# Optimization experiments

Hardware: AMD Instinct MI355X
Metric: run time of the kernel (lower is better)

Reference implementation:

```python
import jax, jax.numpy as jnp
import numpy as np

EMB = 1024
HEADS = 16
HEAD_DIM = EMB // HEADS


def setup_inputs() -> dict:
    key = jax.random.key(0)
    ks = jax.random.split(key, 12)
    B, S = 4, 2048
    scale = 1.0 / np.sqrt(EMB)
    inp = {
        'values': jax.random.normal(ks[0], (B, S, EMB), jnp.float32),
        'keys': jax.random.normal(ks[1], (B, S, EMB), jnp.float32),
        'query': jax.random.normal(ks[2], (B, S, EMB), jnp.float32),
        'Wv': jax.random.normal(ks[3], (EMB, EMB), jnp.float32) * scale,
        'bv': jnp.zeros((EMB,), jnp.float32),
        'Wk': jax.random.normal(ks[4], (EMB, EMB), jnp.float32) * scale,
        'bk': jnp.zeros((EMB,), jnp.float32),
        'Wq': jax.random.normal(ks[5], (EMB, EMB), jnp.float32) * scale,
        'bq': jnp.zeros((EMB,), jnp.float32),
        'Wo': jax.random.normal(ks[6], (EMB, EMB), jnp.float32) * scale,
        'bo': jnp.zeros((EMB,), jnp.float32),
    }
    return inp


def reference(values, keys, query, Wv, bv, Wk, bk, Wq, bq, Wo, bo):
    B, S, _ = values.shape
    # Linear projections (torch Linear: x @ W.T + b)
    v = values @ Wv.T + bv
    k = keys @ Wk.T + bk
    q = query @ Wq.T + bq
    # Reshape to (B, S, H, D) -- NOTE: original does NOT transpose heads,
    # so attention is computed across the HEAD axis per position.
    v = v.reshape(B, S, HEADS, HEAD_DIM)
    k = k.reshape(B, S, HEADS, HEAD_DIM)
    q = q.reshape(B, S, HEADS, HEAD_DIM)
    # (B,S,H,D) @ (B,S,D,H) -> (B,S,H,H) head-head scores
    scores = jnp.einsum('bshd,bsgd->bshg', q, k) * (HEAD_DIM ** -0.5)
    attn = jax.nn.softmax(scores, axis=-1)
    # (B,S,H,H) @ (B,S,H,D) -> (B,S,H,D)
    out = jnp.einsum('bshg,bsgd->bshd', attn, v)
    out = out.reshape(B, S, EMB)
    return out @ Wo.T + bo
```

## Files before the change

### kernel.cpp

```cpp
#include <hip/hip_runtime.h>
#include <stdint.h>

#define EMB 1024
#define LROW 40

typedef unsigned short u16;
typedef __attribute__((ext_vector_type(8))) unsigned short u16x8;
typedef __attribute__((ext_vector_type(8))) __bf16 bf16x8;
typedef __attribute__((ext_vector_type(4))) float f32x4;

__device__ __forceinline__ u16 f2bf(float f) {
  union { float f; uint32_t u; } x; x.f = f;
  uint32_t u = x.u;
  u += 0x7fff + ((u >> 16) & 1u);
  return (u16)(u >> 16);
}

__device__ __forceinline__ bf16x8 cvt8(float4 a, float4 b) {
  bf16x8 r;
  r[0] = (__bf16)a.x; r[1] = (__bf16)a.y; r[2] = (__bf16)a.z; r[3] = (__bf16)a.w;
  r[4] = (__bf16)b.x; r[5] = (__bf16)b.y; r[6] = (__bf16)b.z; r[7] = (__bf16)b.w;
  return r;
}

__device__ __forceinline__ void gl16(const u16* g, u16* l) {
  __builtin_amdgcn_global_load_lds(
      (const __attribute__((address_space(1))) void*)g,
      (__attribute__((address_space(3))) void*)l, 16, 0, 0);
}

__device__ __forceinline__ int xcd_logical(int orig, int nwg) {
  return (orig & 7) * (nwg >> 3) + (orig >> 3);
}

__global__ __launch_bounds__(256) void cvtw_kernel(
    const float* __restrict__ s0, u16* __restrict__ d0,
    const float* __restrict__ s1, u16* __restrict__ d1,
    const float* __restrict__ s2, u16* __restrict__ d2,
    const float* __restrict__ s3, u16* __restrict__ d3)
{
  const float* s; u16* d;
  switch (blockIdx.y) {
    case 0:  s = s0; d = d0; break;
    case 1:  s = s1; d = d1; break;
    case 2:  s = s2; d = d2; break;
    default: s = s3; d = d3; break;
  }
  const size_t i = (size_t)blockIdx.x * 256 + threadIdx.x;
  const float4* f = (const float4*)(s + i * 8);
  const float4 lo = f[0], hi = f[1];
  *(bf16x8*)(d + i * 8) = cvt8(lo, hi);
}

__global__ __launch_bounds__(256, 3) void qkv_fused_kernel(
    const float* __restrict__ Vx, const float* __restrict__ Kx,
    const float* __restrict__ Qx, const u16* __restrict__ Wb,
    const float* __restrict__ Bv, const float* __restrict__ Bk,
    const float* __restrict__ Bq,
    u16* __restrict__ cv, u16* __restrict__ ck, u16* __restrict__ cq,
    int N, int K, int M)
{
  __shared__ __attribute__((aligned(16))) u16 Al[2][128 * 32];
  __shared__ __attribute__((aligned(16))) u16 Bl[2][128 * 32];

  const int nwg = (N >> 7) * (M >> 7) * 3;
  const int logical = xcd_logical(blockIdx.x, nwg);
  const int per_z = (N >> 7) * (M >> 7);
  const int z = logical / per_z;
  const int rem = logical - z * per_z;
  const int nbx = N >> 7;
  const int by = rem / nbx, bx = rem - by * nbx;

  const float* X; const u16* W; const float* Bias; u16* C;
  switch (z) {
    case 0:  X = Vx; W = Wb;                   Bias = Bv; C = cv; break;
    case 1:  X = Kx; W = Wb + EMB * EMB;       Bias = Bk; C = ck; break;
    default: X = Qx; W = Wb + 2 * EMB * EMB;   Bias = Bq; C = cq; break;
  }

  const int tid  = threadIdx.x;
  const int lane = tid & 63;
  const int w    = tid >> 6;
  const int wm = w >> 1, wn = w & 1;
  const int r16 = lane & 15, quad = lane >> 4;
  const int bm = by * 128, bn = bx * 128;

  const int s0 = tid, s1 = tid + 256;
  const int r0 = s0 >> 2, c0 = s0 & 3;
  const int r1 = s1 >> 2, c1 = s1 & 3;
  const int lA0 = r0 * 32 + ((c0 ^ ((r0 >> 1) & 3)) * 8);
  const int lA1 = r1 * 32 + ((c1 ^ ((r1 >> 1) & 3)) * 8);
  const size_t xo0 = (size_t)(bm + r0) * K + c0 * 8;
  const size_t xo1 = (size_t)(bm + r1) * K + c1 * 8;

  const int bs0 = w * 64 + lane, bs1 = bs0 + 256;
  const int br0 = bs0 >> 2, bc0 = ((bs0 & 3) ^ ((br0 >> 1) & 3)) * 8;
  const int br1 = bs1 >> 2, bc1 = ((bs1 & 3) ^ ((br1 >> 1) & 3)) * 8;
  const u16* srcB0 = W + (size_t)(bn + br0) * K + bc0;
  const u16* srcB1 = W + (size_t)(bn + br1) * K + bc1;
  const int dB0o = (w * 64) * 8, dB1o = dB0o + 256 * 8;

  const int swz = (quad ^ ((r16 >> 1) & 3)) * 8;
  int offA[4], offB[4];
#pragma unroll
  for (int t = 0; t < 4; t++) {
    offA[t] = (wm * 64 + t * 16 + r16) * 32 + swz;
    offB[t] = (wn * 64 + t * 16 + r16) * 32 + swz;
  }

  f32x4 acc[4][4];
#pragma unroll
  for (int i = 0; i < 4; i++)
#pragma unroll
    for (int j = 0; j < 4; j++)
      acc[i][j] = f32x4{0.f, 0.f, 0.f, 0.f};

  float4 xa0 = *(const float4*)(X + xo0), xa1 = *(const float4*)(X + xo0 + 4);
  float4 xb0 = *(const float4*)(X + xo1), xb1 = *(const float4*)(X + xo1 + 4);
  *(bf16x8*)&Al[0][lA0] = cvt8(xa0, xa1);
  *(bf16x8*)&Al[0][lA1] = cvt8(xb0, xb1);
  gl16(srcB0, &Bl[0][dB0o]);
  gl16(srcB1, &Bl[0][dB1o]);
  __builtin_amdgcn_sched_barrier(0);
  xa0 = *(const float4*)(X + xo0 + 32); xa1 = *(const float4*)(X + xo0 + 36);
  xb0 = *(const float4*)(X + xo1 + 32); xb1 = *(const float4*)(X + xo1 + 36);
  asm volatile("s_waitcnt vmcnt(4) lgkmcnt(0)\n\ts_barrier" ::: "memory");

  for (int k0 = 0; k0 < K; k0 += 32) {
    const int cur = (k0 >> 5) & 1, nxt = cur ^ 1;
    const int kn  = (k0 + 32) & (K - 1);
    const int kn2 = (k0 + 64) & (K - 1);

    *(bf16x8*)&Al[nxt][lA0] = cvt8(xa0, xa1);
    *(bf16x8*)&Al[nxt][lA1] = cvt8(xb0, xb1);
    gl16(srcB0 + kn, &Bl[nxt][dB0o]);
    gl16(srcB1 + kn, &Bl[nxt][dB1o]);
    __builtin_amdgcn_sched_barrier(0);
    xa0 = *(const float4*)(X + xo0 + kn2); xa1 = *(const float4*)(X + xo0 + kn2 + 4);
    xb0 = *(const float4*)(X + xo1 + kn2); xb1 = *(const float4*)(X + xo1 + kn2 + 4);

    bf16x8 a[4], b[4];
#pragma unroll
    for (int t = 0; t < 4; t++) a[t] = *(const bf16x8*)&Al[cur][offA[t]];
#pragma unroll
    for (int t = 0; t < 4; t++) b[t] = *(const bf16x8*)&Bl[cur][offB[t]];
    asm volatile("s_waitcnt lgkmcnt(0)" ::: "memory");
    __builtin_amdgcn_sched_barrier(0);

#pragma unroll
    for (int tm = 0; tm < 4; tm++)
#pragma unroll
      for (int tn = 0; tn < 4; tn++)
        acc[tm][tn] = __builtin_amdgcn_mfma_f32_16x16x32_bf16(a[tm], b[tn], acc[tm][tn], 0, 0, 0);

    asm volatile("s_waitcnt vmcnt(4)\n\ts_barrier" ::: "memory");
  }

#pragma unroll
  for (int tn = 0; tn < 4; tn++) {
    const int col = bn + wn * 64 + tn * 16 + r16;
    const float bias = Bias[col];
#pragma unroll
    for (int tm = 0; tm < 4; tm++) {
      const int row0 = bm + wm * 64 + tm * 16 + quad * 4;
#pragma unroll
      for (int r = 0; r < 4; r++)
        C[(size_t)(row0 + r) * N + col] = f2bf(acc[tm][tn][r] + bias);
    }
  }
}

__global__ __launch_bounds__(256, 3) void out_gemm_kernel(
    const u16* __restrict__ X, const u16* __restrict__ W,
    const float* __restrict__ Bias, float* __restrict__ C, int N, int K, int M)
{
  __shared__ __attribute__((aligned(16))) u16 Al[2][128 * 32];
  __shared__ __attribute__((aligned(16))) u16 Bl[2][128 * 32];

  const int nwg = (N >> 7) * (M >> 7);
  const int logical = xcd_logical(blockIdx.x, nwg);
  const int nbx = N >> 7;
  const int by = logical / nbx, bx = logical - by * nbx;

  const int tid  = threadIdx.x;
  const int lane = tid & 63;
  const int w    = tid >> 6;
  const int wm = w >> 1, wn = w & 1;
  const int r16 = lane & 15, quad = lane >> 4;
  const int bm = by * 128, bn = bx * 128;

  const int s0 = w * 64 + lane, s1 = s0 + 256;
  const int r0 = s0 >> 2, c0 = ((s0 & 3) ^ ((r0 >> 1) & 3)) * 8;
  const int r1 = s1 >> 2, c1 = ((s1 & 3) ^ ((r1 >> 1) & 3)) * 8;

  const u16* srcA0 = X + (size_t)(bm + r0) * K + c0;
  const u16* srcA1 = X + (size_t)(bm + r1) * K + c1;
  const u16* srcB0 = W + (size_t)(bn + r0) * K + c0;
  const u16* srcB1 = W + (size_t)(bn + r1) * K + c1;

  const int dA0o = (w * 64) * 8, dA1o = dA0o + 256 * 8;

  const int swz = (quad ^ ((r16 >> 1) & 3)) * 8;
  int offA[4], offB[4];
#pragma unroll
  for (int t = 0; t < 4; t++) {
    offA[t] = (wm * 64 + t * 16 + r16) * 32 + swz;
    offB[t] = (wn * 64 + t * 16 + r16) * 32 + swz;
  }

  f32x4 acc[4][4];
#pragma unroll
  for (int i = 0; i < 4; i++)
#pragma unroll
    for (int j = 0; j < 4; j++)
      acc[i][j] = f32x4{0.f, 0.f, 0.f, 0.f};

  gl16(srcA0, &Al[0][dA0o]);
  gl16(srcA1, &Al[0][dA1o]);
  gl16(srcB0, &Bl[0][dA0o]);
  gl16(srcB1, &Bl[0][dA1o]);
  asm volatile("s_waitcnt vmcnt(0)\n\ts_barrier" ::: "memory");

  for (int k0 = 0; k0 < K; k0 += 32) {
    const int cur = (k0 >> 5) & 1, nxt = cur ^ 1;
    const int kn = (k0 + 32) & (K - 1);

    gl16(srcA0 + kn, &Al[nxt][dA0o]);
    gl16(srcA1 + kn, &Al[nxt][dA1o]);
    gl16(srcB0 + kn, &Bl[nxt][dA0o]);
    gl16(srcB1 + kn, &Bl[nxt][dA1o]);

    bf16x8 a[4], b[4];
#pragma unroll
    for (int t = 0; t < 4; t++) a[t] = *(const bf16x8*)&Al[cur][offA[t]];
#pragma unroll
    for (int t = 0; t < 4; t++) b[t] = *(const bf16x8*)&Bl[cur][offB[t]];
    asm volatile("s_waitcnt lgkmcnt(0)" ::: "memory");
    __builtin_amdgcn_sched_barrier(0);

#pragma unroll
    for (int tm = 0; tm < 4; tm++)
#pragma unroll
      for (int tn = 0; tn < 4; tn++)
        acc[tm][tn] = __builtin_amdgcn_mfma_f32_16x16x32_bf16(a[tm], b[tn], acc[tm][tn], 0, 0, 0);

    asm volatile("s_waitcnt vmcnt(0)\n\ts_barrier" ::: "memory");
  }

#pragma unroll
  for (int tn = 0; tn < 4; tn++) {
    const int col = bn + wn * 64 + tn * 16 + r16;
    const float bias = Bias[col];
#pragma unroll
    for (int tm = 0; tm < 4; tm++) {
      const int row0 = bm + wm * 64 + tm * 16 + quad * 4;
#pragma unroll
      for (int r = 0; r < 4; r++)
        C[(size_t)(row0 + r) * N + col] = acc[tm][tn][r] + bias;
    }
  }
}

__global__ __launch_bounds__(256, 4) void attn_heads_kernel(
    const u16* Q, const u16* Km, const u16* V, u16* O)
{
  __shared__ __attribute__((aligned(16))) u16 P[4][16 * LROW];
  __shared__ __attribute__((aligned(16))) u16 VT[4][64 * LROW];

  const int tid = threadIdx.x, lane = tid & 63, w = tid >> 6;
  const int r16 = lane & 15, quad = lane >> 4;
  const size_t base = ((size_t)blockIdx.x * 4 + w) * EMB;

  const bf16x8 aq0 = *(const bf16x8*)&Q[base + r16 * 64 + quad * 8];
  const bf16x8 aq1 = *(const bf16x8*)&Q[base + r16 * 64 + 32 + quad * 8];
  const bf16x8 bk0 = *(const bf16x8*)&Km[base + r16 * 64 + quad * 8];
  const bf16x8 bk1 = *(const bf16x8*)&Km[base + r16 * 64 + 32 + quad * 8];

  const u16x8 v0 = *(const u16x8*)&V[base + lane * 16];
  const u16x8 v1 = *(const u16x8*)&V[base + lane * 16 + 8];
  const u16x8 z8 = {0, 0, 0, 0, 0, 0, 0, 0};
  *(u16x8*)&VT[w][lane * LROW + 16] = z8;
  *(u16x8*)&VT[w][lane * LROW + 24] = z8;
  const int g = lane >> 2, dbase = (lane & 3) * 16;
#pragma unroll
  for (int i = 0; i < 8; i++) {
    VT[w][(dbase + i) * LROW + g]     = v0[i];
    VT[w][(dbase + 8 + i) * LROW + g] = v1[i];
  }

  f32x4 s = f32x4{0.f, 0.f, 0.f, 0.f};
  s = __builtin_amdgcn_mfma_f32_16x16x32_bf16(aq0, bk0, s, 0, 0, 0);
  s = __builtin_amdgcn_mfma_f32_16x16x32_bf16(aq1, bk1, s, 0, 0, 0);

  float p[4];
#pragma unroll
  for (int r = 0; r < 4; r++) {
    float v = s[r] * 0.125f;
    float m = v;
#pragma unroll
    for (int d = 8; d; d >>= 1) m = fmaxf(m, __shfl_xor(m, d, 16));
    float e = __expf(v - m);
    float sum = e;
#pragma unroll
    for (int d = 8; d; d >>= 1) sum += __shfl_xor(sum, d, 16);
    p[r] = e / sum;
  }

#pragma unroll
  for (int r = 0; r < 4; r++) {
    P[w][(quad * 4 + r) * LROW + r16]      = f2bf(p[r]);
    P[w][(quad * 4 + r) * LROW + 16 + r16] = 0;
  }
  __syncthreads();

  const bf16x8 pa = *(const bf16x8*)&P[w][r16 * LROW + quad * 8];

#pragma unroll
  for (int c = 0; c < 4; c++) {
    const bf16x8 bvv = *(const bf16x8*)&VT[w][(c * 16 + r16) * LROW + quad * 8];
    f32x4 o = f32x4{0.f, 0.f, 0.f, 0.f};
    o = __builtin_amdgcn_mfma_f32_16x16x32_bf16(pa, bvv, o, 0, 0, 0);
#pragma unroll
    for (int r = 0; r < 4; r++)
      O[base + (size_t)(quad * 4 + r) * 64 + c * 16 + r16] = f2bf(o[r]);
  }
}

extern "C" void kernel_launch(void* const* d_in, const int* in_sizes, int n_in,
                              void* d_out, int out_size, void* d_ws, size_t ws_size,
                              hipStream_t stream)
{
  const float* values = (const float*)d_in[0];
  const float* keys   = (const float*)d_in[1];
  const float* query  = (const float*)d_in[2];
  const float* Wv = (const float*)d_in[3];
  const float* bv = (const float*)d_in[4];
  const float* Wk = (const float*)d_in[5];
  const float* bk = (const float*)d_in[6];
  const float* Wq = (const float*)d_in[7];
  const float* bq = (const float*)d_in[8];
  const float* Wo = (const float*)d_in[9];
  const float* bo = (const float*)d_in[10];

  const int M = in_sizes[0] / EMB;
  const int N = EMB, K = EMB;

  u16* q    = (u16*)d_ws;
  u16* kbuf = q + (size_t)M * EMB;
  u16* v    = (u16*)d_out;
  u16* wb   = v + (size_t)M * EMB;
  u16* ao   = q;

  const size_t base_ws = (size_t)2 * M * EMB * sizeof(u16);
  const bool wo_in_ws = ws_size >= base_ws + (size_t)EMB * EMB * sizeof(u16);
  u16* wob = wo_in_ws ? kbuf + (size_t)M * EMB : kbuf;

  dim3 blk(256, 1, 1);
  dim3 cwg(EMB * EMB / 8 / 256, wo_in_ws ? 4 : 3, 1);

  hipLaunchKernelGGL(cvtw_kernel, cwg, blk, 0, stream,
                     Wv, wb, Wk, wb + EMB * EMB, Wq, wb + 2 * EMB * EMB, Wo, wob);
  hipLaunchKernelGGL(qkv_fused_kernel, dim3((N / 128) * (M / 128) * 3, 1, 1), blk, 0, stream,
                     values, keys, query, wb, bv, bk, bq, v, kbuf, q, N, K, M);
  hipLaunchKernelGGL(attn_heads_kernel, dim3(M / 4, 1, 1), blk, 0, stream,
                     q, kbuf, v, ao);
  if (!wo_in_ws)
    hipLaunchKernelGGL(cvtw_kernel, dim3(EMB * EMB / 8 / 256, 1, 1), blk, 0, stream,
                       Wo, wob, (const float*)nullptr, (u16*)nullptr,
                       (const float*)nullptr, (u16*)nullptr,
                       (const float*)nullptr, (u16*)nullptr);
  hipLaunchKernelGGL(out_gemm_kernel, dim3((N / 128) * (M / 128), 1, 1), blk, 0, stream,
                     ao, wob, bo, (float*)d_out, N, K, M);
}
```

Measured before the change: 282.7 us.

## Stagger K-loop start phase per tile and raise occupancy launch bounds

Each GEMM workgroup now starts its K reduction at a rotated offset derived from its row tile (and projection index), wrapping around K. The aim is to spread concurrent blocks across different K slices so they stop hitting the same memory channels and weight lines at the same moment. Launch bounds for the QKV, output GEMM and attention kernels are raised to request higher occupancy. The higher bounds may force register spilling or cap accumulator registers, and the rotation assumes K/32 is a power of two.

```diff
diff --git a/kernel.cpp b/kernel.cpp
--- a/kernel.cpp
+++ b/kernel.cpp
@@ -52,7 +52,7 @@
   *(bf16x8*)(d + i * 8) = cvt8(lo, hi);
 }
 
-__global__ __launch_bounds__(256, 3) void qkv_fused_kernel(
+__global__ __launch_bounds__(256, 5) void qkv_fused_kernel(
     const float* __restrict__ Vx, const float* __restrict__ Kx,
     const float* __restrict__ Qx, const u16* __restrict__ Wb,
     const float* __restrict__ Bv, const float* __restrict__ Bk,
@@ -85,6 +85,10 @@
   const int r16 = lane & 15, quad = lane >> 4;
   const int bm = by * 128, bn = bx * 128;
 
+  const int NSTEP = K >> 5;
+  const int SM = NSTEP - 1;
+  const int ph = (by * 3 + z * 21) & SM;
+
   const int s0 = tid, s1 = tid + 256;
   const int r0 = s0 >> 2, c0 = s0 & 3;
   const int r1 = s1 >> 2, c1 = s1 & 3;
@@ -115,21 +119,23 @@
     for (int j = 0; j < 4; j++)
       acc[i][j] = f32x4{0.f, 0.f, 0.f, 0.f};
 
-  float4 xa0 = *(const float4*)(X + xo0), xa1 = *(const float4*)(X + xo0 + 4);
-  float4 xb0 = *(const float4*)(X + xo1), xb1 = *(const float4*)(X + xo1 + 4);
+  const int kP0 = ph << 5;
+  const int kP1 = ((ph + 1) & SM) << 5;
+  float4 xa0 = *(const float4*)(X + xo0 + kP0), xa1 = *(const float4*)(X + xo0 + kP0 + 4);
+  float4 xb0 = *(const float4*)(X + xo1 + kP0), xb1 = *(const float4*)(X + xo1 + kP0 + 4);
   *(bf16x8*)&Al[0][lA0] = cvt8(xa0, xa1);
   *(bf16x8*)&Al[0][lA1] = cvt8(xb0, xb1);
-  gl16(srcB0, &Bl[0][dB0o]);
-  gl16(srcB1, &Bl[0][dB1o]);
+  gl16(srcB0 + kP0, &Bl[0][dB0o]);
+  gl16(srcB1 + kP0, &Bl[0][dB1o]);
   __builtin_amdgcn_sched_barrier(0);
-  xa0 = *(const float4*)(X + xo0 + 32); xa1 = *(const float4*)(X + xo0 + 36);
-  xb0 = *(const float4*)(X + xo1 + 32); xb1 = *(const float4*)(X + xo1 + 36);
+  xa0 = *(const float4*)(X + xo0 + kP1); xa1 = *(const float4*)(X + xo0 + kP1 + 4);
+  xb0 = *(const float4*)(X + xo1 + kP1); xb1 = *(const float4*)(X + xo1 + kP1 + 4);
   asm volatile("s_waitcnt vmcnt(4) lgkmcnt(0)\n\ts_barrier" ::: "memory");
 
-  for (int k0 = 0; k0 < K; k0 += 32) {
-    const int cur = (k0 >> 5) & 1, nxt = cur ^ 1;
-    const int kn  = (k0 + 32) & (K - 1);
-    const int kn2 = (k0 + 64) & (K - 1);
+  for (int it = 0; it < NSTEP; ++it) {
+    const int cur = it & 1, nxt = cur ^ 1;
+    const int kn  = ((it + 1 + ph) & SM) << 5;
+    const int kn2 = ((it + 2 + ph) & SM) << 5;
 
     *(bf16x8*)&Al[nxt][lA0] = cvt8(xa0, xa1);
     *(bf16x8*)&Al[nxt][lA1] = cvt8(xb0, xb1);
@@ -170,7 +176,7 @@
   }
 }
 
-__global__ __launch_bounds__(256, 3) void out_gemm_kernel(
+__global__ __launch_bounds__(256, 5) void out_gemm_kernel(
     const u16* __restrict__ X, const u16* __restrict__ W,
     const float* __restrict__ Bias, float* __restrict__ C, int N, int K, int M)
 {
@@ -189,6 +195,10 @@
   const int r16 = lane & 15, quad = lane >> 4;
   const int bm = by * 128, bn = bx * 128;
 
+  const int NSTEP = K >> 5;
+  const int SM = NSTEP - 1;
+  const int ph = (by * 3) & SM;
+
   const int s0 = w * 64 + lane, s1 = s0 + 256;
   const int r0 = s0 >> 2, c0 = ((s0 & 3) ^ ((r0 >> 1) & 3)) * 8;
   const int r1 = s1 >> 2, c1 = ((s1 & 3) ^ ((r1 >> 1) & 3)) * 8;
@@ -215,15 +225,16 @@
     for (int j = 0; j < 4; j++)
       acc[i][j] = f32x4{0.f, 0.f, 0.f, 0.f};
 
-  gl16(srcA0, &Al[0][dA0o]);
-  gl16(srcA1, &Al[0][dA1o]);
-  gl16(srcB0, &Bl[0][dA0o]);
-  gl16(srcB1, &Bl[0][dA1o]);
+  const int kP0 = ph << 5;
+  gl16(srcA0 + kP0, &Al[0][dA0o]);
+  gl16(srcA1 + kP0, &Al[0][dA1o]);
+  gl16(srcB0 + kP0, &Bl[0][dA0o]);
+  gl16(srcB1 + kP0, &Bl[0][dA1o]);
   asm volatile("s_waitcnt vmcnt(0)\n\ts_barrier" ::: "memory");
 
-  for (int k0 = 0; k0 < K; k0 += 32) {
-    const int cur = (k0 >> 5) & 1, nxt = cur ^ 1;
-    const int kn = (k0 + 32) & (K - 1);
+  for (int it = 0; it < NSTEP; ++it) {
+    const int cur = it & 1, nxt = cur ^ 1;
+    const int kn = ((it + 1 + ph) & SM) << 5;
 
     gl16(srcA0 + kn, &Al[nxt][dA0o]);
     gl16(srcA1 + kn, &Al[nxt][dA1o]);
@@ -261,7 +272,7 @@
   }
 }
 
-__global__ __launch_bounds__(256, 4) void attn_heads_kernel(
+__global__ __launch_bounds__(256, 6) void attn_heads_kernel(
     const u16* Q, const u16* Km, const u16* V, u16* O)
 {
   __shared__ __attribute__((aligned(16))) u16 P[4][16 * LROW];
```

Measured after the change: 885.9 us. +213.3%, slower.

## Triple-buffer LDS tiles in QKV and output GEMMs for deeper prefetch

Applied to the files above, without the earlier changes.

Converts the QKV projection and output projection GEMMs from double- to triple-buffered shared-memory staging. Global-to-LDS loads are issued two k-steps ahead, and the waitcnt thresholds are relaxed so loads for the next step stay in flight across the barrier. The goal is to hide global memory latency better. In exchange each block uses more LDS, which may reduce occupancy, since launch bounds request 3 blocks per CU.

```diff
diff --git a/kernel.cpp b/kernel.cpp
--- a/kernel.cpp
+++ b/kernel.cpp
@@ -61,7 +61,7 @@
     int N, int K, int M)
 {
   __shared__ __attribute__((aligned(16))) u16 Al[2][128 * 32];
-  __shared__ __attribute__((aligned(16))) u16 Bl[2][128 * 32];
+  __shared__ __attribute__((aligned(16))) u16 Bl[3][128 * 32];
 
   const int nwg = (N >> 7) * (M >> 7) * 3;
   const int logical = xcd_logical(blockIdx.x, nwg);
@@ -85,6 +85,9 @@
   const int r16 = lane & 15, quad = lane >> 4;
   const int bm = by * 128, bn = bx * 128;
 
+  const int NSTEP = K >> 5;
+  const int SM = NSTEP - 1;
+
   const int s0 = tid, s1 = tid + 256;
   const int r0 = s0 >> 2, c0 = s0 & 3;
   const int r1 = s1 >> 2, c1 = s1 & 3;
@@ -117,33 +120,38 @@
 
   float4 xa0 = *(const float4*)(X + xo0), xa1 = *(const float4*)(X + xo0 + 4);
   float4 xb0 = *(const float4*)(X + xo1), xb1 = *(const float4*)(X + xo1 + 4);
+  gl16(srcB0, &Bl[0][dB0o]);
+  gl16(srcB1, &Bl[0][dB1o]);
+  gl16(srcB0 + 32, &Bl[1][dB0o]);
+  gl16(srcB1 + 32, &Bl[1][dB1o]);
+  __builtin_amdgcn_sched_barrier(0);
   *(bf16x8*)&Al[0][lA0] = cvt8(xa0, xa1);
   *(bf16x8*)&Al[0][lA1] = cvt8(xb0, xb1);
-  gl16(srcB0, &Bl[0][dB0o]);
-  gl16(srcB1, &Bl[0][dB1o]);
   __builtin_amdgcn_sched_barrier(0);
   xa0 = *(const float4*)(X + xo0 + 32); xa1 = *(const float4*)(X + xo0 + 36);
   xb0 = *(const float4*)(X + xo1 + 32); xb1 = *(const float4*)(X + xo1 + 36);
-  asm volatile("s_waitcnt vmcnt(4) lgkmcnt(0)\n\ts_barrier" ::: "memory");
-
-  for (int k0 = 0; k0 < K; k0 += 32) {
-    const int cur = (k0 >> 5) & 1, nxt = cur ^ 1;
-    const int kn  = (k0 + 32) & (K - 1);
-    const int kn2 = (k0 + 64) & (K - 1);
-
-    *(bf16x8*)&Al[nxt][lA0] = cvt8(xa0, xa1);
-    *(bf16x8*)&Al[nxt][lA1] = cvt8(xb0, xb1);
-    gl16(srcB0 + kn, &Bl[nxt][dB0o]);
-    gl16(srcB1 + kn, &Bl[nxt][dB1o]);
+  asm volatile("s_waitcnt vmcnt(6) lgkmcnt(0)\n\ts_barrier" ::: "memory");
+
+  int brd = 0;
+  for (int it = 0; it < NSTEP; ++it) {
+    const int acur = it & 1, anxt = acur ^ 1;
+    const int bwr = (brd == 0) ? 2 : brd - 1;
+    const int kn2 = ((it + 2) & SM) << 5;
+
+    gl16(srcB0 + kn2, &Bl[bwr][dB0o]);
+    gl16(srcB1 + kn2, &Bl[bwr][dB1o]);
+    __builtin_amdgcn_sched_barrier(0);
+    *(bf16x8*)&Al[anxt][lA0] = cvt8(xa0, xa1);
+    *(bf16x8*)&Al[anxt][lA1] = cvt8(xb0, xb1);
     __builtin_amdgcn_sched_barrier(0);
     xa0 = *(const float4*)(X + xo0 + kn2); xa1 = *(const float4*)(X + xo0 + kn2 + 4);
     xb0 = *(const float4*)(X + xo1 + kn2); xb1 = *(const float4*)(X + xo1 + kn2 + 4);
 
     bf16x8 a[4], b[4];
 #pragma unroll
-    for (int t = 0; t < 4; t++) a[t] = *(const bf16x8*)&Al[cur][offA[t]];
-#pragma unroll
-    for (int t = 0; t < 4; t++) b[t] = *(const bf16x8*)&Bl[cur][offB[t]];
+    for (int t = 0; t < 4; t++) a[t] = *(const bf16x8*)&Al[acur][offA[t]];
+#pragma unroll
+    for (int t = 0; t < 4; t++) b[t] = *(const bf16x8*)&Bl[brd][offB[t]];
     asm volatile("s_waitcnt lgkmcnt(0)" ::: "memory");
     __builtin_amdgcn_sched_barrier(0);
 
@@ -153,7 +161,8 @@
       for (int tn = 0; tn < 4; tn++)
         acc[tm][tn] = __builtin_amdgcn_mfma_f32_16x16x32_bf16(a[tm], b[tn], acc[tm][tn], 0, 0, 0);
 
-    asm volatile("s_waitcnt vmcnt(4)\n\ts_barrier" ::: "memory");
+    asm volatile("s_waitcnt vmcnt(6)\n\ts_barrier" ::: "memory");
+    brd = (brd == 2) ? 0 : brd + 1;
   }
 
 #pragma unroll
@@ -174,8 +183,8 @@
     const u16* __restrict__ X, const u16* __restrict__ W,
     const float* __restrict__ Bias, float* __restrict__ C, int N, int K, int M)
 {
-  __shared__ __attribute__((aligned(16))) u16 Al[2][128 * 32];
-  __shared__ __attribute__((aligned(16))) u16 Bl[2][128 * 32];
+  __shared__ __attribute__((aligned(16))) u16 Al[3][128 * 32];
+  __shared__ __attribute__((aligned(16))) u16 Bl[3][128 * 32];
 
   const int nwg = (N >> 7) * (M >> 7);
   const int logical = xcd_logical(blockIdx.x, nwg);
@@ -189,6 +198,9 @@
   const int r16 = lane & 15, quad = lane >> 4;
   const int bm = by * 128, bn = bx * 128;
 
+  const int NSTEP = K >> 5;
+  const int SM = NSTEP - 1;
+
   const int s0 = w * 64 + lane, s1 = s0 + 256;
   const int r0 = s0 >> 2, c0 = ((s0 & 3) ^ ((r0 >> 1) & 3)) * 8;
   const int r1 = s1 >> 2, c1 = ((s1 & 3) ^ ((r1 >> 1) & 3)) * 8;
@@ -219,22 +231,27 @@
   gl16(srcA1, &Al[0][dA1o]);
   gl16(srcB0, &Bl[0][dA0o]);
   gl16(srcB1, &Bl[0][dA1o]);
-  asm volatile("s_waitcnt vmcnt(0)\n\ts_barrier" ::: "memory");
-
-  for (int k0 = 0; k0 < K; k0 += 32) {
-    const int cur = (k0 >> 5) & 1, nxt = cur ^ 1;
-    const int kn = (k0 + 32) & (K - 1);
-
-    gl16(srcA0 + kn, &Al[nxt][dA0o]);
-    gl16(srcA1 + kn, &Al[nxt][dA1o]);
-    gl16(srcB0 + kn, &Bl[nxt][dA0o]);
-    gl16(srcB1 + kn, &Bl[nxt][dA1o]);
+  gl16(srcA0 + 32, &Al[1][dA0o]);
+  gl16(srcA1 + 32, &Al[1][dA1o]);
+  gl16(srcB0 + 32, &Bl[1][dA0o]);
+  gl16(srcB1 + 32, &Bl[1][dA1o]);
+  asm volatile("s_waitcnt vmcnt(4)\n\ts_barrier" ::: "memory");
+
+  int rd = 0;
+  for (int it = 0; it < NSTEP; ++it) {
+    const int wr = (rd == 0) ? 2 : rd - 1;
+    const int kn2 = ((it + 2) & SM) << 5;
+
+    gl16(srcA0 + kn2, &Al[wr][dA0o]);
+    gl16(srcA1 + kn2, &Al[wr][dA1o]);
+    gl16(srcB0 + kn2, &Bl[wr][dA0o]);
+    gl16(srcB1 + kn2, &Bl[wr][dA1o]);
 
     bf16x8 a[4], b[4];
 #pragma unroll
-    for (int t = 0; t < 4; t++) a[t] = *(const bf16x8*)&Al[cur][offA[t]];
-#pragma unroll
-    for (int t = 0; t < 4; t++) b[t] = *(const bf16x8*)&Bl[cur][offB[t]];
+    for (int t = 0; t < 4; t++) a[t] = *(const bf16x8*)&Al[rd][offA[t]];
+#pragma unroll
+    for (int t = 0; t < 4; t++) b[t] = *(const bf16x8*)&Bl[rd][offB[t]];
     asm volatile("s_waitcnt lgkmcnt(0)" ::: "memory");
     __builtin_amdgcn_sched_barrier(0);
 
@@ -244,7 +261,8 @@
       for (int tn = 0; tn < 4; tn++)
         acc[tm][tn] = __builtin_amdgcn_mfma_f32_16x16x32_bf16(a[tm], b[tn], acc[tm][tn], 0, 0, 0);
 
-    asm volatile("s_waitcnt vmcnt(0)\n\ts_barrier" ::: "memory");
+    asm volatile("s_waitcnt vmcnt(4)\n\ts_barrier" ::: "memory");
+    rd = (rd == 2) ? 0 : rd + 1;
   }
 
 #pragma unroll
```

Result: faster. 270.1 us (-4.5%).
